# Optimization experiments

Hardware: AMD Instinct MI355X
Metric: run time of the kernel (lower is better)

## Reference

```python
import jax, jax.numpy as jnp
import numpy as np


def setup_inputs() -> dict:
    key = jax.random.key(0)
    ks = jax.random.split(key, 8)
    b, l, d, n = 2, 4096, 1024, 16
    s = 0.02
    return {
        "x": jax.random.normal(ks[0], (b, l, d), dtype=jnp.float32),
        "W1": jax.random.normal(ks[1], (d, d), dtype=jnp.float32) * s,
        "b1": jnp.zeros((d,), dtype=jnp.float32),
        "W2": jax.random.normal(ks[2], (n, d), dtype=jnp.float32) * s,
        "b2": jnp.zeros((n,), dtype=jnp.float32),
        "W3": jax.random.normal(ks[3], (n, d), dtype=jnp.float32) * s,
        "b3": jnp.zeros((n,), dtype=jnp.float32),
        "A": jax.random.normal(ks[4], (d, n), dtype=jnp.float32) * s,
    }


def reference(x, W1, b1, W2, b2, W3, b3, A):
    # Faithful to the torch S6.forward as written:
    #   B = fc2(x); C = fc3(x); delta = softplus(fc1(x))
    #   dB = einsum('bld,bln->bldn', delta, B)
    #   h  = dA * 0 + x[..., None] * dB          (h starts at zeros, no scan)
    #   y  = einsum('bln,bldn->bld', C, h)
    # which collapses exactly to y = x * delta * sum_n(C * B).
    # dA = exp(einsum('bld,dn->bldn', delta, A)) is multiplied by zeros and
    # therefore never influences the output (A is a dead parameter here).
    B = jnp.einsum('bld,nd->bln', x, W2) + b2          # (b, l, n)
    C = jnp.einsum('bld,nd->bln', x, W3) + b3          # (b, l, n)
    delta = jax.nn.softplus(jnp.einsum('bld,ed->ble', x, W1) + b1)  # (b, l, d)
    cb = jnp.sum(C * B, axis=-1)                        # (b, l) = sum_n C*B
    y = x * delta * cb[..., None]                       # (b, l, d)
    return y
```

## Files before the change

kernel.cpp:

```cpp
#include <hip/hip_runtime.h>
#include <hip/hip_bf16.h>
#include <stdint.h>

typedef __attribute__((ext_vector_type(8))) short short8;
typedef __attribute__((ext_vector_type(4))) float f32x4;
typedef __attribute__((ext_vector_type(4))) unsigned short us4;

static __device__ __forceinline__ unsigned short f2bf(float f) {
    __hip_bfloat16 h = __float2bfloat16(f);
    union { __hip_bfloat16 h; unsigned short u; } v; v.h = h;
    return v.u;
}
static __device__ __forceinline__ float bf2f(unsigned short h) {
    union { uint32_t u; float f; } v; v.u = ((uint32_t)h) << 16;
    return v.f;
}

static __device__ __forceinline__ short8 cvt8(float4 a, float4 b) {
    short8 r;
    r[0] = (short)f2bf(a.x); r[1] = (short)f2bf(a.y);
    r[2] = (short)f2bf(a.z); r[3] = (short)f2bf(a.w);
    r[4] = (short)f2bf(b.x); r[5] = (short)f2bf(b.y);
    r[6] = (short)f2bf(b.z); r[7] = (short)f2bf(b.w);
    return r;
}

__global__ __launch_bounds__(256) void cb_fused(
    const float* __restrict__ x,
    const float* __restrict__ W1,
    const float* __restrict__ W2,
    const float* __restrict__ b2,
    const float* __restrict__ W3,
    const float* __restrict__ b3,
    unsigned short* __restrict__ xb,
    unsigned short* __restrict__ w1b,
    float* __restrict__ cbo)
{
    const int bid = blockIdx.x;
    const int t = threadIdx.x;

    {
        const float4* w4 = (const float4*)W1;
        const int base = bid * 512 + t;
#pragma unroll
        for (int i = 0; i < 2; ++i) {
            float4 v = w4[base + i * 256];
            us4 r = { f2bf(v.x), f2bf(v.y), f2bf(v.z), f2bf(v.w) };
            *(us4*)&w1b[(size_t)(base + i * 256) * 4] = r;
        }
    }

    __shared__ float red[4][2][16][16];

    const int wave = t >> 6, lane = t & 63;
    const int r0 = bid * 16;
    const int rrow = lane & 15;
    const int klane = (lane >> 4) * 8;
    const size_t xrow = (size_t)(r0 + rrow) * 1024;
    const int k0 = wave * 256;

    f32x4 accB = {0.f, 0.f, 0.f, 0.f};
    f32x4 accC = {0.f, 0.f, 0.f, 0.f};

#pragma unroll
    for (int ks = 0; ks < 256; ks += 32) {
        const int k = k0 + ks + klane;
        float4 xa = *(const float4*)&x[xrow + k];
        float4 xc = *(const float4*)&x[xrow + k + 4];
        short8 af = cvt8(xa, xc);
        *(short8*)&xb[xrow + k] = af;
        float4 w2a = *(const float4*)&W2[(size_t)rrow * 1024 + k];
        float4 w2c = *(const float4*)&W2[(size_t)rrow * 1024 + k + 4];
        float4 w3a = *(const float4*)&W3[(size_t)rrow * 1024 + k];
        float4 w3c = *(const float4*)&W3[(size_t)rrow * 1024 + k + 4];
        short8 w2f = cvt8(w2a, w2c);
        short8 w3f = cvt8(w3a, w3c);
        accB = __builtin_amdgcn_mfma_f32_16x16x32_bf16(af, w2f, accB, 0, 0, 0);
        accC = __builtin_amdgcn_mfma_f32_16x16x32_bf16(af, w3f, accC, 0, 0, 0);
    }

#pragma unroll
    for (int j = 0; j < 4; ++j) {
        red[wave][0][(lane >> 4) * 4 + j][lane & 15] = accB[j];
        red[wave][1][(lane >> 4) * 4 + j][lane & 15] = accC[j];
    }
    __syncthreads();

    if (wave == 0) {
        const int n = lane & 15;
        const float b2v = b2[n], b3v = b3[n];
        float prod[4];
#pragma unroll
        for (int j = 0; j < 4; ++j) {
            const int row = (lane >> 4) * 4 + j;
            float Bv = red[0][0][row][n] + red[1][0][row][n]
                     + red[2][0][row][n] + red[3][0][row][n] + b2v;
            float Cv = red[0][1][row][n] + red[1][1][row][n]
                     + red[2][1][row][n] + red[3][1][row][n] + b3v;
            prod[j] = Bv * Cv;
        }
#pragma unroll
        for (int off = 1; off < 16; off <<= 1)
#pragma unroll
            for (int j = 0; j < 4; ++j)
                prod[j] += __shfl_xor(prod[j], off, 64);
        if ((lane & 15) == 0) {
#pragma unroll
            for (int j = 0; j < 4; ++j)
                cbo[r0 + (lane >> 4) * 4 + j] = prod[j];
        }
    }
}

__global__ __launch_bounds__(256, 2) void gemm_kernel(
    const unsigned short* __restrict__ xb,
    const unsigned short* __restrict__ w1b,
    const float* __restrict__ b1,
    const float* __restrict__ cb,
    float* __restrict__ y)
{
    __shared__ unsigned short As[2][128 * 64];
    __shared__ unsigned short Bs[2][128 * 64];

    const int wg = blockIdx.x;
    const int nid = (wg & 7) * 64 + (wg >> 3);
    const int row0 = (nid >> 3) * 128;
    const int col0 = (nid & 7) * 128;

    const int t = threadIdx.x;
    const int wid = t >> 6, lane = t & 63;
    const int wm = wid >> 1, wn = wid & 1;

    const int lrow = lane >> 3;
    const int gslot = (lane & 7) ^ lrow;

    f32x4 acc[4][4];
#pragma unroll
    for (int m = 0; m < 4; ++m)
#pragma unroll
        for (int n = 0; n < 4; ++n)
            acc[m][n] = (f32x4){0.f, 0.f, 0.f, 0.f};

    auto STAGE = [&](int b, int kt) {
#pragma unroll
        for (int p = 0; p < 4; ++p) {
            const int grp = p * 4 + wid;
            const int row = grp * 8 + lrow;
            const int gc = kt + gslot * 8;
            const unsigned short* ga = &xb[(size_t)(row0 + row) * 1024 + gc];
            const unsigned short* gb = &w1b[(size_t)(col0 + row) * 1024 + gc];
            __builtin_amdgcn_global_load_lds(
                (const __attribute__((address_space(1))) void*)ga,
                (__attribute__((address_space(3))) void*)&As[b][grp * 512 + lane * 8], 16, 0, 0);
            __builtin_amdgcn_global_load_lds(
                (const __attribute__((address_space(1))) void*)gb,
                (__attribute__((address_space(3))) void*)&Bs[b][grp * 512 + lane * 8], 16, 0, 0);
        }
    };

    STAGE(0, 0);
    asm volatile("s_waitcnt vmcnt(0)" ::: "memory");
    __builtin_amdgcn_s_barrier();
    __builtin_amdgcn_sched_barrier(0);

    const int ro = lane & 15;
    const int sh = lane >> 4;

    for (int tk = 0; tk < 16; ++tk) {
        const int cur = tk & 1;
        if (tk < 15) {
            STAGE(cur ^ 1, (tk + 1) * 64);
            asm volatile("s_waitcnt vmcnt(8)" ::: "memory");
        } else {
            asm volatile("s_waitcnt vmcnt(0)" ::: "memory");
        }
        __builtin_amdgcn_s_barrier();
        __builtin_amdgcn_sched_barrier(0);

        short8 af[2][4], bfr[2][4];
#pragma unroll
        for (int ks = 0; ks < 2; ++ks) {
            const int s = ks * 4 + sh;
#pragma unroll
            for (int m = 0; m < 4; ++m) {
                const int ar = wm * 64 + m * 16 + ro;
                af[ks][m]  = *(const short8*)&As[cur][ar * 64 + ((s ^ (ro & 7)) << 3)];
                const int br = wn * 64 + m * 16 + ro;
                bfr[ks][m] = *(const short8*)&Bs[cur][br * 64 + ((s ^ (ro & 7)) << 3)];
            }
        }
        __builtin_amdgcn_s_setprio(1);
#pragma unroll
        for (int ks = 0; ks < 2; ++ks)
#pragma unroll
            for (int m = 0; m < 4; ++m)
#pragma unroll
                for (int n = 0; n < 4; ++n)
                    acc[m][n] = __builtin_amdgcn_mfma_f32_16x16x32_bf16(af[ks][m], bfr[ks][n], acc[m][n], 0, 0, 0);
        __builtin_amdgcn_s_setprio(0);

        asm volatile("s_waitcnt lgkmcnt(0)" ::: "memory");
        __builtin_amdgcn_s_barrier();
        __builtin_amdgcn_sched_barrier(0);
    }

#pragma unroll
    for (int m = 0; m < 4; ++m) {
        const int grow_base = row0 + wm * 64 + m * 16 + (lane >> 4) * 4;
#pragma unroll
        for (int n = 0; n < 4; ++n) {
            const int gcol = col0 + wn * 64 + n * 16 + (lane & 15);
            const float bv = b1[gcol];
#pragma unroll
            for (int j = 0; j < 4; ++j) {
                const int grow = grow_base + j;
                const float v = acc[m][n][j] + bv;
                const float sp = (v > 15.f) ? v : __logf(1.f + __expf(v));
                const size_t off = (size_t)grow * 1024 + gcol;
                y[off] = bf2f(xb[off]) * sp * cb[grow];
            }
        }
    }
}

extern "C" void kernel_launch(void* const* d_in, const int* in_sizes, int n_in,
                              void* d_out, int out_size, void* d_ws, size_t ws_size,
                              hipStream_t stream) {
    const float* x  = (const float*)d_in[0];
    const float* W1 = (const float*)d_in[1];
    const float* b1 = (const float*)d_in[2];
    const float* W2 = (const float*)d_in[3];
    const float* b2 = (const float*)d_in[4];
    const float* W3 = (const float*)d_in[5];
    const float* b3 = (const float*)d_in[6];

    float* y = (float*)d_out;

    unsigned short* xb  = (unsigned short*)d_ws;
    unsigned short* w1b = xb + (size_t)8192 * 1024;
    float* cbuf = (float*)(w1b + (size_t)1024 * 1024);

    cb_fused<<<512, 256, 0, stream>>>(x, W1, W2, b2, W3, b3, xb, w1b, cbuf);
    gemm_kernel<<<512, 256, 0, stream>>>(xb, w1b, b1, cbuf, y);
}
```

Before: 46.32 us.

## Fold B/C projections into main GEMM and simplify prep to pure conversion

The first kernel becomes a plain grid-stride fp32-to-bf16 conversion of x, W1, W2 and W3. The B and C projections move into the main GEMM: each wave multiplies its already-loaded A fragments against W2 (wn==0) or W3 (wn==1) fragments read straight from global memory. The partial results are exchanged through LDS and reduced with shuffles to form cb per row. This removes the MFMA and reduction work from the prep kernel. The cost is redundant B/C computation in each of the 8 column tiles and an extra global load plus 8 MFMAs per k-step in the GEMM.

Result: no change. 47.09 us (+1.7%).

```diff
diff --git a/kernel.cpp b/kernel.cpp
--- a/kernel.cpp
+++ b/kernel.cpp
@@ -16,107 +16,40 @@
     return v.f;
 }
 
-static __device__ __forceinline__ short8 cvt8(float4 a, float4 b) {
-    short8 r;
-    r[0] = (short)f2bf(a.x); r[1] = (short)f2bf(a.y);
-    r[2] = (short)f2bf(a.z); r[3] = (short)f2bf(a.w);
-    r[4] = (short)f2bf(b.x); r[5] = (short)f2bf(b.y);
-    r[6] = (short)f2bf(b.z); r[7] = (short)f2bf(b.w);
-    return r;
-}
-
-__global__ __launch_bounds__(256) void cb_fused(
+__global__ __launch_bounds__(256) void convert_k(
     const float* __restrict__ x,
     const float* __restrict__ W1,
     const float* __restrict__ W2,
-    const float* __restrict__ b2,
     const float* __restrict__ W3,
-    const float* __restrict__ b3,
     unsigned short* __restrict__ xb,
     unsigned short* __restrict__ w1b,
-    float* __restrict__ cbo)
+    unsigned short* __restrict__ w2b,
+    unsigned short* __restrict__ w3b)
 {
-    const int bid = blockIdx.x;
-    const int t = threadIdx.x;
-
-    {
-        const float4* w4 = (const float4*)W1;
-        const int base = bid * 512 + t;
-#pragma unroll
-        for (int i = 0; i < 2; ++i) {
-            float4 v = w4[base + i * 256];
-            us4 r = { f2bf(v.x), f2bf(v.y), f2bf(v.z), f2bf(v.w) };
-            *(us4*)&w1b[(size_t)(base + i * 256) * 4] = r;
-        }
-    }
-
-    __shared__ float red[4][2][16][16];
-
-    const int wave = t >> 6, lane = t & 63;
-    const int r0 = bid * 16;
-    const int rrow = lane & 15;
-    const int klane = (lane >> 4) * 8;
-    const size_t xrow = (size_t)(r0 + rrow) * 1024;
-    const int k0 = wave * 256;
-
-    f32x4 accB = {0.f, 0.f, 0.f, 0.f};
-    f32x4 accC = {0.f, 0.f, 0.f, 0.f};
-
-#pragma unroll
-    for (int ks = 0; ks < 256; ks += 32) {
-        const int k = k0 + ks + klane;
-        float4 xa = *(const float4*)&x[xrow + k];
-        float4 xc = *(const float4*)&x[xrow + k + 4];
-        short8 af = cvt8(xa, xc);
-        *(short8*)&xb[xrow + k] = af;
-        float4 w2a = *(const float4*)&W2[(size_t)rrow * 1024 + k];
-        float4 w2c = *(const float4*)&W2[(size_t)rrow * 1024 + k + 4];
-        float4 w3a = *(const float4*)&W3[(size_t)rrow * 1024 + k];
-        float4 w3c = *(const float4*)&W3[(size_t)rrow * 1024 + k + 4];
-        short8 w2f = cvt8(w2a, w2c);
-        short8 w3f = cvt8(w3a, w3c);
-        accB = __builtin_amdgcn_mfma_f32_16x16x32_bf16(af, w2f, accB, 0, 0, 0);
-        accC = __builtin_amdgcn_mfma_f32_16x16x32_bf16(af, w3f, accC, 0, 0, 0);
-    }
-
-#pragma unroll
-    for (int j = 0; j < 4; ++j) {
-        red[wave][0][(lane >> 4) * 4 + j][lane & 15] = accB[j];
-        red[wave][1][(lane >> 4) * 4 + j][lane & 15] = accC[j];
-    }
-    __syncthreads();
-
-    if (wave == 0) {
-        const int n = lane & 15;
-        const float b2v = b2[n], b3v = b3[n];
-        float prod[4];
-#pragma unroll
-        for (int j = 0; j < 4; ++j) {
-            const int row = (lane >> 4) * 4 + j;
-            float Bv = red[0][0][row][n] + red[1][0][row][n]
-                     + red[2][0][row][n] + red[3][0][row][n] + b2v;
-            float Cv = red[0][1][row][n] + red[1][1][row][n]
-                     + red[2][1][row][n] + red[3][1][row][n] + b3v;
-            prod[j] = Bv * Cv;
-        }
-#pragma unroll
-        for (int off = 1; off < 16; off <<= 1)
-#pragma unroll
-            for (int j = 0; j < 4; ++j)
-                prod[j] += __shfl_xor(prod[j], off, 64);
-        if ((lane & 15) == 0) {
-#pragma unroll
-            for (int j = 0; j < 4; ++j)
-                cbo[r0 + (lane >> 4) * 4 + j] = prod[j];
-        }
+    const int N1 = 2097152;
+    const int N2 = 262144;
+    const int N3 = 4096;
+    const int NT = N1 + N2 + 2 * N3;
+    for (int i = blockIdx.x * 256 + threadIdx.x; i < NT; i += 2048 * 256) {
+        const float4* src; unsigned short* dst; int off;
+        if (i < N1)            { src = (const float4*)x;  dst = xb;  off = i; }
+        else if (i < N1 + N2)  { src = (const float4*)W1; dst = w1b; off = i - N1; }
+        else if (i < N1 + N2 + N3) { src = (const float4*)W2; dst = w2b; off = i - N1 - N2; }
+        else                   { src = (const float4*)W3; dst = w3b; off = i - N1 - N2 - N3; }
+        float4 v = src[off];
+        us4 r = { f2bf(v.x), f2bf(v.y), f2bf(v.z), f2bf(v.w) };
+        *(us4*)&dst[(size_t)off * 4] = r;
     }
 }
 
 __global__ __launch_bounds__(256, 2) void gemm_kernel(
     const unsigned short* __restrict__ xb,
     const unsigned short* __restrict__ w1b,
+    const unsigned short* __restrict__ w2b,
+    const unsigned short* __restrict__ w3b,
     const float* __restrict__ b1,
-    const float* __restrict__ cb,
+    const float* __restrict__ b2,
+    const float* __restrict__ b3,
     float* __restrict__ y)
 {
     __shared__ unsigned short As[2][128 * 64];
@@ -134,12 +67,17 @@
     const int lrow = lane >> 3;
     const int gslot = (lane & 7) ^ lrow;
 
+    const unsigned short* wsel = (wn == 0) ? w2b : w3b;
+
     f32x4 acc[4][4];
 #pragma unroll
     for (int m = 0; m < 4; ++m)
 #pragma unroll
         for (int n = 0; n < 4; ++n)
             acc[m][n] = (f32x4){0.f, 0.f, 0.f, 0.f};
+    f32x4 accW[4];
+#pragma unroll
+    for (int m = 0; m < 4; ++m) accW[m] = (f32x4){0.f, 0.f, 0.f, 0.f};
 
     auto STAGE = [&](int b, int kt) {
 #pragma unroll
@@ -168,8 +106,15 @@
 
     for (int tk = 0; tk < 16; ++tk) {
         const int cur = tk & 1;
+        const int kt = tk * 64;
+
+        short8 wf[2];
+        wf[0] = *(const short8*)&wsel[(size_t)ro * 1024 + kt + sh * 8];
+        wf[1] = *(const short8*)&wsel[(size_t)ro * 1024 + kt + 32 + sh * 8];
+        __builtin_amdgcn_sched_barrier(0);
+
         if (tk < 15) {
-            STAGE(cur ^ 1, (tk + 1) * 64);
+            STAGE(cur ^ 1, kt + 64);
             asm volatile("s_waitcnt vmcnt(8)" ::: "memory");
         } else {
             asm volatile("s_waitcnt vmcnt(0)" ::: "memory");
@@ -197,11 +142,50 @@
 #pragma unroll
                 for (int n = 0; n < 4; ++n)
                     acc[m][n] = __builtin_amdgcn_mfma_f32_16x16x32_bf16(af[ks][m], bfr[ks][n], acc[m][n], 0, 0, 0);
+#pragma unroll
+        for (int ks = 0; ks < 2; ++ks)
+#pragma unroll
+            for (int m = 0; m < 4; ++m)
+                accW[m] = __builtin_amdgcn_mfma_f32_16x16x32_bf16(af[ks][m], wf[ks], accW[m], 0, 0, 0);
         __builtin_amdgcn_s_setprio(0);
 
         asm volatile("s_waitcnt lgkmcnt(0)" ::: "memory");
         __builtin_amdgcn_s_barrier();
         __builtin_amdgcn_sched_barrier(0);
+    }
+
+    float* exch = (float*)(&As[0][0]);
+    float* exB = exch;
+    float* exC = exch + 2048;
+    {
+        float* dst = (wn == 0) ? exB : exC;
+        const int n = lane & 15;
+#pragma unroll
+        for (int m = 0; m < 4; ++m)
+#pragma unroll
+            for (int j = 0; j < 4; ++j)
+                dst[(wm * 64 + m * 16 + (lane >> 4) * 4 + j) * 16 + n] = accW[m][j];
+    }
+    __syncthreads();
+
+    float cb_loc[4][4];
+    {
+        const int n = lane & 15;
+        const float b2v = b2[n], b3v = b3[n];
+#pragma unroll
+        for (int m = 0; m < 4; ++m)
+#pragma unroll
+            for (int j = 0; j < 4; ++j) {
+                const int r = wm * 64 + m * 16 + (lane >> 4) * 4 + j;
+                const float Bv = (wn == 0) ? accW[m][j] : exB[r * 16 + n];
+                const float Cv = (wn == 0) ? exC[r * 16 + n] : accW[m][j];
+                float p = (Bv + b2v) * (Cv + b3v);
+                p += __shfl_xor(p, 1, 64);
+                p += __shfl_xor(p, 2, 64);
+                p += __shfl_xor(p, 4, 64);
+                p += __shfl_xor(p, 8, 64);
+                cb_loc[m][j] = p;
+            }
     }
 
 #pragma unroll
@@ -217,7 +201,7 @@
                 const float v = acc[m][n][j] + bv;
                 const float sp = (v > 15.f) ? v : __logf(1.f + __expf(v));
                 const size_t off = (size_t)grow * 1024 + gcol;
-                y[off] = bf2f(xb[off]) * sp * cb[grow];
+                y[off] = bf2f(xb[off]) * sp * cb_loc[m][j];
             }
         }
     }
@@ -238,8 +222,9 @@
 
     unsigned short* xb  = (unsigned short*)d_ws;
     unsigned short* w1b = xb + (size_t)8192 * 1024;
-    float* cbuf = (float*)(w1b + (size_t)1024 * 1024);
-
-    cb_fused<<<512, 256, 0, stream>>>(x, W1, W2, b2, W3, b3, xb, w1b, cbuf);
-    gemm_kernel<<<512, 256, 0, stream>>>(xb, w1b, b1, cbuf, y);
-}
+    unsigned short* w2b = w1b + (size_t)1024 * 1024;
+    unsigned short* w3b = w2b + (size_t)16 * 1024;
+
+    convert_k<<<2048, 256, 0, stream>>>(x, W1, W2, W3, xb, w1b, w2b, w3b);
+    gemm_kernel<<<512, 256, 0, stream>>>(xb, w1b, w2b, w3b, b1, b2, b3, y);
+}
```
